# Kernel tuning notes

Hardware: AMD Instinct MI355X
Metric: run time of the kernel (lower is better)

Reference implementation:

```python
import jax, jax.numpy as jnp
import numpy as np

B, S, D, H = 4, 2048, 1024, 16
DK = D // H

def setup_inputs() -> dict:
    key = jax.random.key(0)
    ks = jax.random.split(key, 7)
    f = lambda k, shape: jax.random.normal(k, shape, dtype=jnp.float32)
    return {
        "query": f(ks[0], (B, S, D)),
        "key":   f(ks[1], (B, S, D)),
        "value": f(ks[2], (B, S, D)),
        "w_q": f(ks[3], (D, D)) * (D ** -0.5),
        "w_k": f(ks[4], (D, D)) * (D ** -0.5),
        "w_v": f(ks[5], (D, D)) * (D ** -0.5),
        "w_o": f(ks[6], (D, D)) * (D ** -0.5),
    }

def reference(query, key, value, w_q, w_k, w_v, w_o):
    # Linear layers: y = x @ W^T (torch nn.Linear convention), bias=False
    def split_heads(x):  # [B,S,D] -> [B,H,S,DK]
        return x.reshape(B, S, H, DK).transpose(0, 2, 1, 3)
    Q = split_heads(query @ w_q.T)
    K = split_heads(key @ w_k.T)
    V = split_heads(value @ w_v.T)
    scale = jnp.float32(1.0 / np.sqrt(DK))
    scores = jnp.einsum('bhqd,bhkd->bhqk', Q, K) * scale  # [B,H,Sq,Sk]
    attn = jax.nn.softmax(scores, axis=-1)
    out = jnp.einsum('bhqk,bhkd->bhqd', attn, V)  # [B,H,Sq,DK]
    out = out.transpose(0, 2, 1, 3).reshape(B, S, D)
    return out @ w_o.T
```

## Files before the change

### kernel.cpp

```cpp
#include <hip/hip_runtime.h>
#include <stdint.h>

#define NB 4
#define NS 2048
#define ND 1024
#define NH 16
#define NDK 64
#define NM (NB*NS)

typedef __attribute__((ext_vector_type(8))) short short8;
typedef __attribute__((ext_vector_type(8))) unsigned short ushort8v;
typedef __attribute__((ext_vector_type(4))) unsigned short ushort4v;
typedef __attribute__((ext_vector_type(4))) float f32x4;
typedef __attribute__((ext_vector_type(16))) float f32x16;

__device__ __forceinline__ unsigned short f2bf(float f) {
  union { float f; uint32_t u; } v; v.f = f;
  uint32_t u = v.u;
  return (unsigned short)((u + 0x7FFFu + ((u >> 16) & 1u)) >> 16);
}

__device__ __forceinline__ void gload16(const void* g, void* l) {
  __builtin_amdgcn_global_load_lds(
      (const __attribute__((address_space(1))) void*)g,
      (__attribute__((address_space(3))) void*)l, 16, 0, 0);
}

__global__ void convert_all(
    const float* __restrict__ x0, const float* __restrict__ x1, const float* __restrict__ x2,
    const float* __restrict__ w0, const float* __restrict__ w1,
    const float* __restrict__ w2, const float* __restrict__ w3,
    unsigned short* __restrict__ ox0, unsigned short* __restrict__ ox1, unsigned short* __restrict__ ox2,
    unsigned short* __restrict__ ow0, unsigned short* __restrict__ ow1,
    unsigned short* __restrict__ ow2, unsigned short* __restrict__ ow3)
{
  const float* src;
  unsigned short* dst;
  size_t i;
  if (blockIdx.y < 3) {
    src = blockIdx.y == 0 ? x0 : (blockIdx.y == 1 ? x1 : x2);
    dst = blockIdx.y == 0 ? ox0 : (blockIdx.y == 1 ? ox1 : ox2);
    i = ((size_t)blockIdx.x * 256 + threadIdx.x) * 8;
  } else {
    if (blockIdx.x >= 2048) return;
    size_t e = ((size_t)blockIdx.x * 256 + threadIdx.x) * 8;
    int which = (int)(e >> 20);
    size_t off = e & ((1u << 20) - 1);
    const float* ws[4] = {w0, w1, w2, w3};
    unsigned short* wd[4] = {ow0, ow1, ow2, ow3};
    src = ws[which]; dst = wd[which]; i = off;
  }
  f32x4 a = *(const f32x4*)(src + i);
  f32x4 b = *(const f32x4*)(src + i + 4);
  ushort8v h;
  h[0]=f2bf(a.x); h[1]=f2bf(a.y); h[2]=f2bf(a.z); h[3]=f2bf(a.w);
  h[4]=f2bf(b.x); h[5]=f2bf(b.y); h[6]=f2bf(b.z); h[7]=f2bf(b.w);
  *(ushort8v*)(dst + i) = h;
}

template<int OUT, int PRESCALE>
__device__ __forceinline__ void gemm_core(
    const unsigned short* __restrict__ A,
    const unsigned short* __restrict__ Bt,
    void* __restrict__ Cout,
    unsigned short* As, unsigned short* Bs)
{
  const int N = ND, K = ND;
  const int tid = threadIdx.x;
  const int lane = tid & 63, wid = tid >> 6;
  const int l15 = lane & 15, lg = lane >> 4;
  const int wr = wid >> 1, wc = wid & 1;
  const int m0 = blockIdx.y * 128, n0 = blockIdx.x * 128;
  const float QSC = 0.125f * 1.44269504088896f;

  f32x4 acc[4][4] = {};

  int arow[4], ach[4];
#pragma unroll
  for (int c = 0; c < 4; ++c) {
    int slot = (wid*4 + c)*64 + lane;
    arow[c] = slot >> 3; ach[c] = slot & 7;
  }

  for (int k0 = 0; k0 < K; k0 += 64) {
#pragma unroll
    for (int c = 0; c < 4; ++c) {
      gload16(A  + (size_t)(m0 + arow[c])*K + k0 + ach[c]*8, As + (wid*4 + c)*512);
      gload16(Bt + (size_t)(n0 + arow[c])*K + k0 + ach[c]*8, Bs + (wid*4 + c)*512);
    }
    __syncthreads();
#pragma unroll
    for (int kk = 0; kk < 2; ++kk) {
      short8 af[4], bfr[4];
#pragma unroll
      for (int m = 0; m < 4; ++m)
        af[m] = *(const short8*)(As + (wr*64 + m*16 + l15)*64 + kk*32 + lg*8);
#pragma unroll
      for (int n = 0; n < 4; ++n)
        bfr[n] = *(const short8*)(Bs + (wc*64 + n*16 + l15)*64 + kk*32 + lg*8);
#pragma unroll
      for (int m = 0; m < 4; ++m)
#pragma unroll
        for (int n = 0; n < 4; ++n)
          acc[m][n] = __builtin_amdgcn_mfma_f32_16x16x32_bf16(af[m], bfr[n], acc[m][n], 0, 0, 0);
    }
    __syncthreads();
  }

#pragma unroll
  for (int m = 0; m < 4; ++m)
#pragma unroll
    for (int n = 0; n < 4; ++n)
#pragma unroll
      for (int i = 0; i < 4; ++i) {
        int row = m0 + wr*64 + m*16 + lg*4 + i;
        int col = n0 + wc*64 + n*16 + l15;
        float val = PRESCALE ? acc[m][n][i] * QSC : acc[m][n][i];
        if (OUT == 0)
          ((float*)Cout)[(size_t)row * N + col] = val;
        else if (OUT == 1)
          ((unsigned short*)Cout)[(size_t)row * N + col] = f2bf(val);
        else
          ((unsigned short*)Cout)[((size_t)((row >> 11)*1024 + col))*NS + (row & (NS-1))]
              = f2bf(val);
      }
}

__global__ __launch_bounds__(256) void gemm_qkv(
    const unsigned short* __restrict__ Xq, const unsigned short* __restrict__ Wq, unsigned short* Qb,
    const unsigned short* __restrict__ Xk, const unsigned short* __restrict__ Wk, unsigned short* Kb,
    const unsigned short* __restrict__ Xv, const unsigned short* __restrict__ Wv, unsigned short* VbT)
{
  __shared__ unsigned short As[128*64];
  __shared__ unsigned short Bs[128*64];
  if (blockIdx.z == 0)      gemm_core<1,1>(Xq, Wq, Qb,  As, Bs);
  else if (blockIdx.z == 1) gemm_core<1,0>(Xk, Wk, Kb,  As, Bs);
  else                      gemm_core<2,0>(Xv, Wv, VbT, As, Bs);
}

__global__ __launch_bounds__(256) void gemm_o(
    const unsigned short* __restrict__ A, const unsigned short* __restrict__ Bt, float* C)
{
  __shared__ unsigned short As[128*64];
  __shared__ unsigned short Bs[128*64];
  gemm_core<0,0>(A, Bt, C, As, Bs);
}

__global__ __launch_bounds__(256, 4) void flash_attn(
    const unsigned short* __restrict__ Qb,
    const unsigned short* __restrict__ Kb,
    const unsigned short* __restrict__ VT,
    unsigned short* __restrict__ O)
{
  __shared__ unsigned short Kt[2][64*64];
  __shared__ unsigned short Vt[2][64*64];
  const int tid = threadIdx.x, lane = tid & 63, wid = tid >> 6;
  const int l31 = lane & 31, hi = lane >> 5;
  const int bh = blockIdx.y, b = bh >> 4, h = bh & 15;
  const int q0 = blockIdx.x * 128 + wid * 32;

  const unsigned short* Kp[2]; const unsigned short* Vp[2]; int dofs[2];
#pragma unroll
  for (int p = 0; p < 2; ++p) {
    int slot = tid + p*256;
    int srow = slot >> 3;
    int sch  = ((slot & 7) ^ (srow & 7)) * 8;
    Kp[p] = Kb + ((size_t)(b*NS + srow))*ND + h*64 + sch;
    Vp[p] = VT + (size_t)bh*64*NS + (size_t)srow*NS + sch;
    dofs[p] = slot * 8;
  }

  short8 qf[4];
#pragma unroll
  for (int ks = 0; ks < 4; ++ks)
    qf[ks] = *(const short8*)(Qb + (size_t)(b*NS + q0 + l31)*ND + h*64 + ks*16 + hi*8);

  f32x16 oacc[2] = {};
  float lsum = 0.f;

#pragma unroll
  for (int p = 0; p < 2; ++p) {
    gload16(Kp[p], &Kt[0][dofs[p]]);
    gload16(Vp[p], &Vt[0][dofs[p]]);
  }
  __syncthreads();

  for (int t = 0; t < NS/64; ++t) {
    const int cur = t & 1;
    if (t + 1 < NS/64) {
#pragma unroll
      for (int p = 0; p < 2; ++p) {
        gload16(Kp[p] + (size_t)(t+1)*64*ND, &Kt[cur^1][dofs[p]]);
        gload16(Vp[p] + (t+1)*64,            &Vt[cur^1][dofs[p]]);
      }
    }
    const char* Kc = (const char*)Kt[cur];
    const char* Vc = (const char*)Vt[cur];

    f32x16 st[2] = {};
    __builtin_amdgcn_s_setprio(1);
#pragma unroll
    for (int n = 0; n < 2; ++n) {
      const int r = n*32 + l31;
#pragma unroll
      for (int ks = 0; ks < 4; ++ks) {
        short8 kf = *(const short8*)(Kc + r*128 + (((2*ks + hi)*16) ^ ((r & 7) << 4)));
        st[n] = __builtin_amdgcn_mfma_f32_32x32x16_bf16(kf, qf[ks], st[n], 0, 0, 0);
      }
    }
    __builtin_amdgcn_s_setprio(0);

    float rs = 0.f;
#pragma unroll
    for (int n = 0; n < 2; ++n)
#pragma unroll
      for (int r = 0; r < 16; ++r) {
        float p = __builtin_amdgcn_exp2f(st[n][r]);
        st[n][r] = p;
        rs += p;
      }
    rs += __shfl_xor(rs, 32);
    lsum += rs;

    uint32_t w[2][4][2];
#pragma unroll
    for (int n = 0; n < 2; ++n)
#pragma unroll
      for (int e = 0; e < 4; ++e) {
        asm("v_cvt_pk_bf16_f32 %0, %1, %2"
            : "=v"(w[n][e][0]) : "v"(st[n][4*e+0]), "v"(st[n][4*e+1]));
        asm("v_cvt_pk_bf16_f32 %0, %1, %2"
            : "=v"(w[n][e][1]) : "v"(st[n][4*e+2]), "v"(st[n][4*e+3]));
      }

    short8 pa[2][2];
#pragma unroll
    for (int n = 0; n < 2; ++n)
#pragma unroll
      for (int ksl = 0; ksl < 2; ++ksl) {
        uint32_t a0 = w[n][2*ksl][0], b0 = w[n][2*ksl+1][0];
        uint32_t a1 = w[n][2*ksl][1], b1 = w[n][2*ksl+1][1];
        asm("v_permlane32_swap_b32 %0, %1" : "+v"(a0), "+v"(b0));
        asm("v_permlane32_swap_b32 %0, %1" : "+v"(a1), "+v"(b1));
        union { uint32_t u[4]; short8 s; } f;
        f.u[0] = a0; f.u[1] = a1; f.u[2] = b0; f.u[3] = b1;
        pa[n][ksl] = f.s;
      }

    __builtin_amdgcn_s_setprio(1);
#pragma unroll
    for (int d = 0; d < 2; ++d) {
      const int dr = d*32 + l31;
#pragma unroll
      for (int n = 0; n < 2; ++n)
#pragma unroll
        for (int ksl = 0; ksl < 2; ++ksl) {
          const int g = n*4 + ksl*2 + hi;
          short8 vf = *(const short8*)(Vc + dr*128 + ((g*16) ^ ((dr & 7) << 4)));
          oacc[d] = __builtin_amdgcn_mfma_f32_32x32x16_bf16(pa[n][ksl], vf, oacc[d], 0, 0, 0);
        }
    }
    __builtin_amdgcn_s_setprio(0);
    __syncthreads();
  }

  float linv[16];
#pragma unroll
  for (int r = 0; r < 16; ++r)
    linv[r] = 1.0f / __shfl(lsum, (r & 3) + 8*(r >> 2) + 4*hi);
#pragma unroll
  for (int d = 0; d < 2; ++d)
#pragma unroll
    for (int r = 0; r < 16; ++r) {
      int qrow = q0 + (r & 3) + 8*(r >> 2) + 4*hi;
      O[(size_t)(b*NS + qrow)*ND + h*64 + d*32 + l31] = f2bf(oacc[d][r] * linv[r]);
    }
}

extern "C" void kernel_launch(void* const* d_in, const int* in_sizes, int n_in,
                              void* d_out, int out_size, void* d_ws, size_t ws_size,
                              hipStream_t stream) {
  const float* q  = (const float*)d_in[0];
  const float* k  = (const float*)d_in[1];
  const float* v  = (const float*)d_in[2];
  const float* wq = (const float*)d_in[3];
  const float* wk = (const float*)d_in[4];
  const float* wv = (const float*)d_in[5];
  const float* wo = (const float*)d_in[6];

  unsigned short* Wq = (unsigned short*)d_ws;
  unsigned short* Wk = Wq + (size_t)ND*ND;
  unsigned short* Wv = Wk + (size_t)ND*ND;
  unsigned short* Wo = Wv + (size_t)ND*ND;
  unsigned short* Xq = Wo + (size_t)ND*ND;
  unsigned short* Xk = Xq + (size_t)NM*ND;
  unsigned short* Xv = Xk + (size_t)NM*ND;
  unsigned short* Qb = Xv + (size_t)NM*ND;
  unsigned short* Kb = Qb + (size_t)NM*ND;
  unsigned short* VbT = (unsigned short*)d_out;
  unsigned short* Ob  = Xq;

  convert_all<<<dim3(NM*ND/(256*8), 4), 256, 0, stream>>>(
      q, k, v, wq, wk, wv, wo, Xq, Xk, Xv, Wq, Wk, Wv, Wo);

  gemm_qkv<<<dim3(ND/128, NM/128, 3), 256, 0, stream>>>(Xq, Wq, Qb, Xk, Wk, Kb, Xv, Wv, VbT);

  flash_attn<<<dim3(NS/128, NB*NH), 256, 0, stream>>>(Qb, Kb, VbT, Ob);

  gemm_o<<<dim3(ND/128, NM/128), 256, 0, stream>>>(Ob, Wo, (float*)d_out);
}
```

Measured before the change: 226.6 us.

## Add XCD-aware block swizzle and chunk-major K/V LDS layout in attention

```diff
diff --git a/kernel.cpp b/kernel.cpp
--- a/kernel.cpp
+++ b/kernel.cpp
@@ -24,6 +24,10 @@
   __builtin_amdgcn_global_load_lds(
       (const __attribute__((address_space(1))) void*)g,
       (__attribute__((address_space(3))) void*)l, 16, 0, 0);
+}
+
+__device__ __forceinline__ int xcd_swz(int flat, int nwg) {
+  return (flat & 7) * (nwg >> 3) + (flat >> 3);
 }
 
 __global__ void convert_all(
@@ -63,14 +67,14 @@
     const unsigned short* __restrict__ A,
     const unsigned short* __restrict__ Bt,
     void* __restrict__ Cout,
-    unsigned short* As, unsigned short* Bs)
+    unsigned short* As, unsigned short* Bs,
+    int m0, int n0)
 {
   const int N = ND, K = ND;
   const int tid = threadIdx.x;
   const int lane = tid & 63, wid = tid >> 6;
   const int l15 = lane & 15, lg = lane >> 4;
   const int wr = wid >> 1, wc = wid & 1;
-  const int m0 = blockIdx.y * 128, n0 = blockIdx.x * 128;
   const float QSC = 0.125f * 1.44269504088896f;
 
   f32x4 acc[4][4] = {};
@@ -133,9 +137,13 @@
 {
   __shared__ unsigned short As[128*64];
   __shared__ unsigned short Bs[128*64];
-  if (blockIdx.z == 0)      gemm_core<1,1>(Xq, Wq, Qb,  As, Bs);
-  else if (blockIdx.z == 1) gemm_core<1,0>(Xk, Wk, Kb,  As, Bs);
-  else                      gemm_core<2,0>(Xv, Wv, VbT, As, Bs);
+  int flat = (blockIdx.z * 64 + blockIdx.y) * 8 + blockIdx.x;
+  int swz = xcd_swz(flat, 1536);
+  int z = swz >> 9, y = (swz >> 3) & 63, x = swz & 7;
+  int m0 = y * 128, n0 = x * 128;
+  if (z == 0)      gemm_core<1,1>(Xq, Wq, Qb,  As, Bs, m0, n0);
+  else if (z == 1) gemm_core<1,0>(Xk, Wk, Kb,  As, Bs, m0, n0);
+  else             gemm_core<2,0>(Xv, Wv, VbT, As, Bs, m0, n0);
 }
 
 __global__ __launch_bounds__(256) void gemm_o(
@@ -143,7 +151,9 @@
 {
   __shared__ unsigned short As[128*64];
   __shared__ unsigned short Bs[128*64];
-  gemm_core<0,0>(A, Bt, C, As, Bs);
+  int flat = blockIdx.y * 8 + blockIdx.x;
+  int swz = xcd_swz(flat, 512);
+  gemm_core<0,0>(A, Bt, C, As, Bs, (swz >> 3) * 128, (swz & 7) * 128);
 }
 
 __global__ __launch_bounds__(256, 4) void flash_attn(
@@ -156,17 +166,18 @@
   __shared__ unsigned short Vt[2][64*64];
   const int tid = threadIdx.x, lane = tid & 63, wid = tid >> 6;
   const int l31 = lane & 31, hi = lane >> 5;
-  const int bh = blockIdx.y, b = bh >> 4, h = bh & 15;
-  const int q0 = blockIdx.x * 128 + wid * 32;
+  int flat = blockIdx.y * 16 + blockIdx.x;
+  int swz = xcd_swz(flat, 1024);
+  const int bh = swz >> 4, b = bh >> 4, h = bh & 15;
+  const int q0 = (swz & 15) * 128 + wid * 32;
 
   const unsigned short* Kp[2]; const unsigned short* Vp[2]; int dofs[2];
 #pragma unroll
   for (int p = 0; p < 2; ++p) {
     int slot = tid + p*256;
-    int srow = slot >> 3;
-    int sch  = ((slot & 7) ^ (srow & 7)) * 8;
-    Kp[p] = Kb + ((size_t)(b*NS + srow))*ND + h*64 + sch;
-    Vp[p] = VT + (size_t)bh*64*NS + (size_t)srow*NS + sch;
+    int g = slot >> 6, r = slot & 63;
+    Kp[p] = Kb + ((size_t)(b*NS + r))*ND + h*64 + g*8;
+    Vp[p] = VT + ((size_t)(bh*64 + r))*NS + g*8;
     dofs[p] = slot * 8;
   }
 
@@ -204,7 +215,7 @@
       const int r = n*32 + l31;
 #pragma unroll
       for (int ks = 0; ks < 4; ++ks) {
-        short8 kf = *(const short8*)(Kc + r*128 + (((2*ks + hi)*16) ^ ((r & 7) << 4)));
+        short8 kf = *(const short8*)(Kc + (((2*ks + hi) << 10) + r*16));
         st[n] = __builtin_amdgcn_mfma_f32_32x32x16_bf16(kf, qf[ks], st[n], 0, 0, 0);
       }
     }
@@ -256,7 +267,7 @@
 #pragma unroll
         for (int ksl = 0; ksl < 2; ++ksl) {
           const int g = n*4 + ksl*2 + hi;
-          short8 vf = *(const short8*)(Vc + dr*128 + ((g*16) ^ ((dr & 7) << 4)));
+          short8 vf = *(const short8*)(Vc + ((g << 10) + dr*16));
           oacc[d] = __builtin_amdgcn_mfma_f32_32x32x16_bf16(pa[n][ksl], vf, oacc[d], 0, 0, 0);
         }
     }
@@ -303,9 +314,9 @@
   convert_all<<<dim3(NM*ND/(256*8), 4), 256, 0, stream>>>(
       q, k, v, wq, wk, wv, wo, Xq, Xk, Xv, Wq, Wk, Wv, Wo);
 
-  gemm_qkv<<<dim3(ND/128, NM/128, 3), 256, 0, stream>>>(Xq, Wq, Qb, Xk, Wk, Kb, Xv, Wv, VbT);
-
-  flash_attn<<<dim3(NS/128, NB*NH), 256, 0, stream>>>(Qb, Kb, VbT, Ob);
-
-  gemm_o<<<dim3(ND/128, NM/128), 256, 0, stream>>>(Ob, Wo, (float*)d_out);
-}
+  gemm_qkv<<<dim3(8, 64, 3), 256, 0, stream>>>(Xq, Wq, Qb, Xk, Wk, Kb, Xv, Wv, VbT);
+
+  flash_attn<<<dim3(16, 64), 256, 0, stream>>>(Qb, Kb, VbT, Ob);
+
+  gemm_o<<<dim3(8, 64), 256, 0, stream>>>(Ob, Wo, (float*)d_out);
+}
```

After: 227.2 us. No clear change (+0.2%).
